# Kernel optimization log

Measured on AMD Instinct MI355X. Metric: run time of the kernel, lower is better.

## Reference

```python
import jax, jax.numpy as jnp
import numpy as np

B, N, E = 16, 64, 512
C_IMG = 512
H1, H2, H3 = 256, 128, 64
U, R = 8, 8
BBC = 9
EH1, EH2 = 64, 64
BBOX_POS_MAX = 1024.0
EPS = 1e-5


def setup_inputs():
    key = jax.random.key(0)
    ks = jax.random.split(key, 24)
    f = lambda i, shape, s=0.05: jax.random.normal(ks[i], shape, jnp.float32) * s
    return {
        'roi_features': f(0, (B, N, C_IMG), 1.0),
        'batch_bboxes': jax.random.uniform(ks[1], (B, N, 4)) * BBOX_POS_MAX,
        'batch_directions': jax.random.uniform(ks[2], (B, N, 4)),
        'batch_priorities': jax.random.uniform(ks[3], (B, N)),
        'w1': f(4, (C_IMG, H1)), 'b1': f(5, (H1,)),
        'bn1_g': jnp.ones((H1,)), 'bn1_b': jnp.zeros((H1,)),
        'bn1_m': jnp.zeros((H1,)), 'bn1_v': jnp.ones((H1,)),
        'w2': f(6, (H1, H2)), 'b2': f(7, (H2,)),
        'bn2_g': jnp.ones((H2,)), 'bn2_b': jnp.zeros((H2,)),
        'bn2_m': jnp.zeros((H2,)), 'bn2_v': jnp.ones((H2,)),
        'w3': f(8, (H2, H3)), 'b3': f(9, (H3,)),
        'wn': f(10, (H3, U)), 'bn_c': f(11, (U,)),
        'we1': f(12, (2 * BBC, EH1)), 'be1': f(13, (EH1,)),
        'we2': f(14, (EH1, EH2)), 'be2': f(15, (EH2,)),
        'wei': f(16, (EH2, R)), 'bei': f(17, (R,)),
        'edge_index': jax.random.randint(ks[18], (B, 2, E), 0, N, dtype=jnp.int32),
    }


def _bn(x, g, b, m, v):
    # BatchNorm1d in eval mode (running stats)
    return (x - m) * jax.lax.rsqrt(v + EPS) * g + b


def _build_see(edge_index):
    # Padded neighbor table replacing edge_index2dict:
    # see[b,n,0] = n, then srcs of edges with dst==n, in original edge order.
    src = edge_index[:, 0, :]                                   # [B,E]
    dst = edge_index[:, 1, :]                                   # [B,E]
    eq = dst[:, :, None] == dst[:, None, :]                     # [B,E,E]
    lower = jnp.tril(jnp.ones((E, E), bool), -1)
    pos = jnp.sum(eq & lower, axis=-1) + 1                      # rank within dst group, +1 for self slot
    see = jnp.zeros((B, N, N), jnp.int32).at[:, :, 0].set(jnp.arange(N, dtype=jnp.int32))
    b_idx = jnp.arange(B)[:, None]
    see = see.at[b_idx, dst, pos].set(src, mode='drop')
    deg = jnp.zeros((B, N), jnp.int32).at[b_idx, dst].add(1)
    count = jnp.minimum(deg + 1, N)
    mask = (jnp.arange(N)[None, None, :] < count[:, :, None]).astype(jnp.float32)  # [B,N,N]
    return see, mask


def _forward(roi_features, batch_bboxes, batch_directions, batch_priorities,
             w1, b1, bn1_g, bn1_b, bn1_m, bn1_v,
             w2, b2, bn2_g, bn2_b, bn2_m, bn2_v,
             w3, b3, wn, bn_c,
             we1, be1, we2, be2, wei, bei, edge_index):
    see, mask = _build_see(edge_index)
    # --- node branch (node_predictor + node_concept_interpreter) ---
    x = roi_features.reshape(B * N, C_IMG)
    x = jax.nn.relu(_bn(x @ w1 + b1, bn1_g, bn1_b, bn1_m, bn1_v))
    x = jax.nn.relu(_bn(x @ w2 + b2, bn2_g, bn2_b, bn2_m, bn2_v))
    x = jax.nn.relu(x @ w3 + b3)
    node_c = jax.nn.sigmoid(x @ wn + bn_c).reshape(B, N, U)
    # get_nlm_unary_concepts: gather per-node neighborhood into dense [B,N,N,U]
    gu = jax.vmap(lambda u, s: u[s])(node_c, see)               # [B,N,N,U]
    node_concepts = (gu * mask[..., None]).reshape(B * N, N, U)
    # --- edge branch ---
    attr = jnp.concatenate([batch_bboxes / BBOX_POS_MAX, batch_directions,
                            batch_priorities[..., None]], axis=-1)  # [B,N,BBC]
    pair = jnp.concatenate([
        jnp.broadcast_to(attr[:, :, None, :], (B, N, N, BBC)),
        jnp.broadcast_to(attr[:, None, :, :], (B, N, N, BBC))], axis=-1).reshape(-1, 2 * BBC)
    e = jax.nn.relu(pair @ we1 + be1)
    e = jax.nn.relu(e @ we2 + be2)
    rel = jax.nn.sigmoid(e @ wei + bei).reshape(B, N, N, R)
    # get_nlm_binary_concepts: rel[b, see[b,n,i], see[b,n,j]] with zero padding
    def per_b(r, s, m):
        g = r[s[:, :, None], s[:, None, :]]                     # [N,N,N,R]
        return g * (m[:, :, None, None] * m[:, None, :, None])
    edge_concepts = jax.vmap(per_b)(rel, see, mask).reshape(B * N, N, N, R)
    return node_concepts, edge_concepts


def reference(roi_features, batch_bboxes, batch_directions, batch_priorities,
              w1, b1, bn1_g, bn1_b, bn1_m, bn1_v,
              w2, b2, bn2_g, bn2_b, bn2_m, bn2_v,
              w3, b3, wn, bn_c,
              we1, be1, we2, be2, wei, bei, edge_index):
    return _forward(roi_features, batch_bboxes, batch_directions, batch_priorities,
                    w1, b1, bn1_g, bn1_b, bn1_m, bn1_v,
                    w2, b2, bn2_g, bn2_b, bn2_m, bn2_v,
                    w3, b3, wn, bn_c,
                    we1, be1, we2, be2, wei, bei, edge_index)
```

## Files before the change

### kernel.cpp

```cpp
#include <hip/hip_runtime.h>
#include <math.h>

#define BB    16
#define NN    64
#define EE    512
#define CIMG  512
#define H1D   256
#define H2D   128
#define H3D   64
#define UD    8
#define RD    8
#define BBCD  9
#define EH1D  64
#define EH2D  64
#define EPSF  1e-5f

typedef float nfloat4 __attribute__((ext_vector_type(4)));

__global__ __launch_bounds__(256) void fusedA_kernel(
    const int* __restrict__ edge_index,
    const float* __restrict__ bboxes,
    const float* __restrict__ dirs,
    const float* __restrict__ prios,
    const float* __restrict__ we1, const float* __restrict__ be1,
    int* __restrict__ see, int* __restrict__ cnt,
    const float* __restrict__ roi,
    const float* __restrict__ w1, const float* __restrict__ b1,
    const float* __restrict__ g1, const float* __restrict__ bt1,
    const float* __restrict__ m1, const float* __restrict__ v1,
    const float* __restrict__ w2, const float* __restrict__ b2,
    const float* __restrict__ g2, const float* __restrict__ bt2,
    const float* __restrict__ m2, const float* __restrict__ v2,
    const float* __restrict__ w3, const float* __restrict__ b3,
    const float* __restrict__ wn, const float* __restrict__ bnc,
    float* __restrict__ node_c,
    const float* __restrict__ we2, const float* __restrict__ be2,
    const float* __restrict__ wei, const float* __restrict__ bei,
    float* __restrict__ rel,
    float* __restrict__ out_edge)
{
    __shared__ union {
        struct {
            int src[EE];
            int dst[EE];
            int see[NN * NN];
        } p;
        struct {
            float part[4096];
            float h1[4][H1D];
            float h2[4][H2D];
            float h3[4][H3D];
        } n;
        struct {
            float e1[NN * 68];
            float qw[NN * EH1D];
            float wei[EH2D * RD];
            float attr[NN][BBCD];
            float we1[2 * BBCD * EH1D];
            float Pi[EH1D];
            float be2[EH2D];
            float bei[RD];
        } e;
    } sm;

    const int t = threadIdx.x;

    if (blockIdx.x >= BB + 256 + BB * NN) {
        const int id = blockIdx.x - (BB + 256 + BB * NN);
        nfloat4* dst = (nfloat4*)(out_edge + (size_t)id * NN * NN * RD);
        const nfloat4 z = {0.f, 0.f, 0.f, 0.f};
        #pragma unroll
        for (int it = 0; it < 16; ++it) {
            int task = it * 256 + t;
            __builtin_nontemporal_store(z, dst + task * 2);
            __builtin_nontemporal_store(z, dst + task * 2 + 1);
        }
        return;
    }

    if (blockIdx.x < BB) {
        const int b = blockIdx.x;
        const int* ei = edge_index + b * 2 * EE;
        for (int e = t; e < EE; e += 256) {
            sm.p.src[e] = ei[e];
            sm.p.dst[e] = ei[EE + e];
        }
        for (int x = t; x < NN * NN; x += 256)
            sm.p.see[x] = ((x & (NN - 1)) == 0) ? (x >> 6) : 0;
        __syncthreads();

        if (t < NN) {
            int pos = 0;
            #pragma unroll 8
            for (int e = 0; e < EE; ++e) {
                if (sm.p.dst[e] == t) {
                    ++pos;
                    if (pos < NN) sm.p.see[t * NN + pos] = sm.p.src[e];
                }
            }
            int c = pos + 1;
            cnt[b * NN + t] = (c < NN) ? c : NN;
        }
        __syncthreads();

        int4* dst4 = (int4*)(see + b * NN * NN);
        const int4* src4 = (const int4*)sm.p.see;
        for (int x = t; x < (NN * NN) / 4; x += 256) dst4[x] = src4[x];
        return;
    }

    if (blockIdx.x >= BB + 256) {
        const int id = blockIdx.x - (BB + 256);
        const int b = id >> 6;
        const int i = id & 63;

        if (t < NN) {
            const float* bbp = bboxes + (b * NN + t) * 4;
            const float* ddp = dirs + (b * NN + t) * 4;
            sm.e.attr[t][0] = bbp[0] * (1.0f / 1024.0f);
            sm.e.attr[t][1] = bbp[1] * (1.0f / 1024.0f);
            sm.e.attr[t][2] = bbp[2] * (1.0f / 1024.0f);
            sm.e.attr[t][3] = bbp[3] * (1.0f / 1024.0f);
            sm.e.attr[t][4] = ddp[0];
            sm.e.attr[t][5] = ddp[1];
            sm.e.attr[t][6] = ddp[2];
            sm.e.attr[t][7] = ddp[3];
            sm.e.attr[t][8] = prios[b * NN + t];
        }
        for (int x = t; x < 2 * BBCD * EH1D; x += 256) sm.e.we1[x] = we1[x];
        {
            const float4* w4 = (const float4*)we2;
            float4* qw4 = (float4*)sm.e.qw;
            #pragma unroll
            for (int x = 0; x < 4; ++x) qw4[x * 256 + t] = w4[x * 256 + t];
        }
        if (t < 128) ((float4*)sm.e.wei)[t] = ((const float4*)wei)[t];
        if (t < EH2D) sm.e.be2[t] = be2[t];
        if (t < RD) sm.e.bei[t] = bei[t];
        __syncthreads();

        if (t < EH1D) {
            float p = be1[t];
            #pragma unroll
            for (int c = 0; c < BBCD; ++c)
                p = fmaf(sm.e.attr[i][c], sm.e.we1[c * EH1D + t], p);
            sm.e.Pi[t] = p;
        }
        __syncthreads();

        {
            const int o = t & 63;
            const int jw = t >> 6;
            #pragma unroll
            for (int jg = 0; jg < 16; ++jg) {
                const int j = jg * 4 + jw;
                float a = sm.e.Pi[o];
                #pragma unroll
                for (int c = 0; c < BBCD; ++c)
                    a = fmaf(sm.e.attr[j][c], sm.e.we1[(BBCD + c) * EH1D + o], a);
                sm.e.e1[j * 68 + o] = fmaxf(0.f, a);
            }
        }
        __syncthreads();

        const int tx = t & 15, ty = t >> 4;
        const int o0 = tx * 4, j0 = ty * 4;
        float acc[4][4];
        #pragma unroll
        for (int r = 0; r < 4; ++r)
            #pragma unroll
            for (int o = 0; o < 4; ++o) acc[r][o] = 0.f;

        #pragma unroll 4
        for (int cg = 0; cg < 16; ++cg) {
            float ev[4][4];
            #pragma unroll
            for (int r = 0; r < 4; ++r) {
                float4 v = *(const float4*)(sm.e.e1 + (j0 + r) * 68 + cg * 4);
                ev[r][0] = v.x; ev[r][1] = v.y; ev[r][2] = v.z; ev[r][3] = v.w;
            }
            #pragma unroll
            for (int q = 0; q < 4; ++q) {
                float4 wv = *(const float4*)(sm.e.qw + (cg * 4 + q) * EH1D + o0);
                #pragma unroll
                for (int r = 0; r < 4; ++r) {
                    acc[r][0] = fmaf(ev[r][q], wv.x, acc[r][0]);
                    acc[r][1] = fmaf(ev[r][q], wv.y, acc[r][1]);
                    acc[r][2] = fmaf(ev[r][q], wv.z, acc[r][2]);
                    acc[r][3] = fmaf(ev[r][q], wv.w, acc[r][3]);
                }
            }
        }

        {
            float4 bv = *(const float4*)(sm.e.be2 + o0);
            #pragma unroll
            for (int r = 0; r < 4; ++r) {
                float4 v;
                v.x = fmaxf(0.f, acc[r][0] + bv.x);
                v.y = fmaxf(0.f, acc[r][1] + bv.y);
                v.z = fmaxf(0.f, acc[r][2] + bv.z);
                v.w = fmaxf(0.f, acc[r][3] + bv.w);
                *(float4*)(sm.e.e1 + (j0 + r) * 68 + o0) = v;
            }
        }
        __syncthreads();

        {
            const int j = t >> 2;
            const int r0 = (t & 3) * 2;
            float a0 = sm.e.bei[r0], a1 = sm.e.bei[r0 + 1];
            const float* e2row = sm.e.e1 + j * 68;
            #pragma unroll
            for (int og = 0; og < 16; ++og) {
                float4 e2v = *(const float4*)(e2row + og * 4);
                float2 w0 = *(const float2*)(sm.e.wei + (og * 4 + 0) * RD + r0);
                float2 w1 = *(const float2*)(sm.e.wei + (og * 4 + 1) * RD + r0);
                float2 w2 = *(const float2*)(sm.e.wei + (og * 4 + 2) * RD + r0);
                float2 w3 = *(const float2*)(sm.e.wei + (og * 4 + 3) * RD + r0);
                a0 = fmaf(e2v.x, w0.x, a0); a1 = fmaf(e2v.x, w0.y, a1);
                a0 = fmaf(e2v.y, w1.x, a0); a1 = fmaf(e2v.y, w1.y, a1);
                a0 = fmaf(e2v.z, w2.x, a0); a1 = fmaf(e2v.z, w2.y, a1);
                a0 = fmaf(e2v.w, w3.x, a0); a1 = fmaf(e2v.w, w3.y, a1);
            }
            float2 o;
            o.x = 1.f / (1.f + expf(-a0));
            o.y = 1.f / (1.f + expf(-a1));
            *(float2*)(rel + ((size_t)id * NN + j) * RD + r0) = o;
        }
        return;
    }

    const int row0 = (blockIdx.x - BB) * 4;
    float* part = sm.n.part;

    {
        const int og = t & 63, kg = t >> 6;
        const float4* w1v = (const float4*)w1;
        const float4* roiv = (const float4*)(roi + (size_t)row0 * CIMG);
        float acc[4][4];
        #pragma unroll
        for (int r = 0; r < 4; ++r)
            #pragma unroll
            for (int c = 0; c < 4; ++c) acc[r][c] = 0.f;

        for (int cq = 0; cq < 32; ++cq) {
            const int c4 = kg * 32 + cq;
            float x[4][4], w[4][4];
            #pragma unroll
            for (int r = 0; r < 4; ++r) {
                float4 v = roiv[r * 128 + c4];
                x[r][0] = v.x; x[r][1] = v.y; x[r][2] = v.z; x[r][3] = v.w;
            }
            #pragma unroll
            for (int q = 0; q < 4; ++q) {
                float4 v = w1v[(size_t)(c4 * 4 + q) * 64 + og];
                w[q][0] = v.x; w[q][1] = v.y; w[q][2] = v.z; w[q][3] = v.w;
            }
            #pragma unroll
            for (int r = 0; r < 4; ++r)
                #pragma unroll
                for (int q = 0; q < 4; ++q)
                    #pragma unroll
                    for (int c = 0; c < 4; ++c)
                        acc[r][c] = fmaf(x[r][q], w[q][c], acc[r][c]);
        }
        #pragma unroll
        for (int r = 0; r < 4; ++r) {
            float4 v = {acc[r][0], acc[r][1], acc[r][2], acc[r][3]};
            *(float4*)(part + (kg * 4 + r) * 256 + og * 4) = v;
        }
    }
    __syncthreads();
    {
        const int o = t;
        const float bias = b1[o];
        const float scale = rsqrtf(v1[o] + EPSF) * g1[o];
        const float beta = bt1[o];
        const float mu = m1[o];
        #pragma unroll
        for (int r = 0; r < 4; ++r) {
            float s = part[(0 * 4 + r) * 256 + o] + part[(1 * 4 + r) * 256 + o]
                    + part[(2 * 4 + r) * 256 + o] + part[(3 * 4 + r) * 256 + o];
            sm.n.h1[r][o] = fmaxf(0.f, (s + bias - mu) * scale + beta);
        }
    }
    __syncthreads();

    {
        const int og = t & 31, kg = t >> 5;
        const float4* w2v = (const float4*)w2;
        float acc[4][4];
        #pragma unroll
        for (int r = 0; r < 4; ++r)
            #pragma unroll
            for (int c = 0; c < 4; ++c) acc[r][c] = 0.f;

        #pragma unroll
        for (int cq = 0; cq < 8; ++cq) {
            const int c4 = kg * 8 + cq;
            float x[4][4], w[4][4];
            #pragma unroll
            for (int r = 0; r < 4; ++r) {
                float4 v = *(const float4*)&sm.n.h1[r][c4 * 4];
                x[r][0] = v.x; x[r][1] = v.y; x[r][2] = v.z; x[r][3] = v.w;
            }
            #pragma unroll
            for (int q = 0; q < 4; ++q) {
                float4 v = w2v[(size_t)(c4 * 4 + q) * 32 + og];
                w[q][0] = v.x; w[q][1] = v.y; w[q][2] = v.z; w[q][3] = v.w;
            }
            #pragma unroll
            for (int r = 0; r < 4; ++r)
                #pragma unroll
                for (int q = 0; q < 4; ++q)
                    #pragma unroll
                    for (int c = 0; c < 4; ++c)
                        acc[r][c] = fmaf(x[r][q], w[q][c], acc[r][c]);
        }
        #pragma unroll
        for (int r = 0; r < 4; ++r) {
            float4 v = {acc[r][0], acc[r][1], acc[r][2], acc[r][3]};
            *(float4*)(part + (kg * 4 + r) * 128 + og * 4) = v;
        }
    }
    __syncthreads();
    {
        const int o = t & 127;
        const int rp = t >> 7;
        const float bias = b2[o];
        const float scale = rsqrtf(v2[o] + EPSF) * g2[o];
        const float beta = bt2[o];
        const float mu = m2[o];
        #pragma unroll
        for (int rr = 0; rr < 2; ++rr) {
            const int r = rp + rr * 2;
            float s = 0.f;
            #pragma unroll
            for (int kg = 0; kg < 8; ++kg) s += part[(kg * 4 + r) * 128 + o];
            sm.n.h2[r][o] = fmaxf(0.f, (s + bias - mu) * scale + beta);
        }
    }
    __syncthreads();

    {
        const int og = t & 15, kg = t >> 4;
        const float4* w3v = (const float4*)w3;
        float acc[4][4];
        #pragma unroll
        for (int r = 0; r < 4; ++r)
            #pragma unroll
            for (int c = 0; c < 4; ++c) acc[r][c] = 0.f;

        #pragma unroll
        for (int cq = 0; cq < 2; ++cq) {
            const int c4 = kg * 2 + cq;
            float x[4][4], w[4][4];
            #pragma unroll
            for (int r = 0; r < 4; ++r) {
                float4 v = *(const float4*)&sm.n.h2[r][c4 * 4];
                x[r][0] = v.x; x[r][1] = v.y; x[r][2] = v.z; x[r][3] = v.w;
            }
            #pragma unroll
            for (int q = 0; q < 4; ++q) {
                float4 v = w3v[(size_t)(c4 * 4 + q) * 16 + og];
                w[q][0] = v.x; w[q][1] = v.y; w[q][2] = v.z; w[q][3] = v.w;
            }
            #pragma unroll
            for (int r = 0; r < 4; ++r)
                #pragma unroll
                for (int q = 0; q < 4; ++q)
                    #pragma unroll
                    for (int c = 0; c < 4; ++c)
                        acc[r][c] = fmaf(x[r][q], w[q][c], acc[r][c]);
        }
        #pragma unroll
        for (int r = 0; r < 4; ++r) {
            float4 v = {acc[r][0], acc[r][1], acc[r][2], acc[r][3]};
            *(float4*)(part + (kg * 4 + r) * 64 + og * 4) = v;
        }
    }
    __syncthreads();
    {
        const int o = t & 63;
        const int r = t >> 6;
        float s = b3[o];
        #pragma unroll
        for (int kg = 0; kg < 16; ++kg) s += part[(kg * 4 + r) * 64 + o];
        sm.n.h3[r][o] = fmaxf(0.f, s);
    }
    __syncthreads();

    if (t < 32) {
        const int o = t & 7, r = t >> 3;
        float a = bnc[o];
        #pragma unroll 8
        for (int c = 0; c < H3D; ++c) a = fmaf(sm.n.h3[r][c], wn[c * UD + o], a);
        node_c[(size_t)(row0 + r) * UD + o] = 1.f / (1.f + expf(-a));
    }
}

__global__ __launch_bounds__(256) void gather_kernel(
    const int* __restrict__ see, const int* __restrict__ cnt,
    const float* __restrict__ node_c, const float* __restrict__ rel,
    float* __restrict__ out_node, float* __restrict__ out_edge)
{
    __shared__ int s_s[NN];

    const int t = threadIdx.x;
    const int bi = blockIdx.x;
    const int b = bi >> 6;
    const int c = cnt[bi];

    if (t < NN) s_s[t] = see[bi * NN + t];
    __syncthreads();

    if (t < NN) {
        const float m = (t < c) ? 1.f : 0.f;
        const float4* src = (const float4*)(node_c + (size_t)(b * NN + s_s[t]) * UD);
        float4 v0 = src[0], v1 = src[1];
        v0.x *= m; v0.y *= m; v0.z *= m; v0.w *= m;
        v1.x *= m; v1.y *= m; v1.z *= m; v1.w *= m;
        float4* dst = (float4*)(out_node + ((size_t)bi * NN + t) * UD);
        dst[0] = v0;
        dst[1] = v1;
    }

    const float* relb = rel + (size_t)b * NN * NN * RD;
    float* outb = out_edge + (size_t)bi * NN * NN * RD;

    const int total = c * c;
    for (int task = t; task < total; task += 256) {
        int j = task / c;
        int k = task - j * c;
        const float4* src =
            (const float4*)(relb + (size_t)(s_s[j] * NN + s_s[k]) * RD);
        float4 v0 = src[0], v1 = src[1];
        float4* dst = (float4*)(outb + ((size_t)j * NN + k) * RD);
        dst[0] = v0;
        dst[1] = v1;
    }
}

extern "C" void kernel_launch(void* const* d_in, const int* in_sizes, int n_in,
                              void* d_out, int out_size, void* d_ws, size_t ws_size,
                              hipStream_t stream)
{
    const float* roi  = (const float*)d_in[0];
    const float* bbox = (const float*)d_in[1];
    const float* dirs = (const float*)d_in[2];
    const float* prio = (const float*)d_in[3];
    const float* w1   = (const float*)d_in[4];
    const float* b1   = (const float*)d_in[5];
    const float* g1   = (const float*)d_in[6];
    const float* bt1  = (const float*)d_in[7];
    const float* m1   = (const float*)d_in[8];
    const float* v1   = (const float*)d_in[9];
    const float* w2   = (const float*)d_in[10];
    const float* b2   = (const float*)d_in[11];
    const float* g2   = (const float*)d_in[12];
    const float* bt2  = (const float*)d_in[13];
    const float* m2   = (const float*)d_in[14];
    const float* v2   = (const float*)d_in[15];
    const float* w3   = (const float*)d_in[16];
    const float* b3   = (const float*)d_in[17];
    const float* wn   = (const float*)d_in[18];
    const float* bnc  = (const float*)d_in[19];
    const float* we1  = (const float*)d_in[20];
    const float* be1  = (const float*)d_in[21];
    const float* we2  = (const float*)d_in[22];
    const float* be2  = (const float*)d_in[23];
    const float* wei  = (const float*)d_in[24];
    const float* bei  = (const float*)d_in[25];
    const int* edge_index = (const int*)d_in[26];

    char* ws = (char*)d_ws;
    int*   see    = (int*)ws;   ws += (size_t)BB * NN * NN * 4;
    int*   cnt    = (int*)ws;   ws += (size_t)BB * NN * 4;
    float* node_c = (float*)ws; ws += (size_t)BB * NN * UD * 4;
    float* rel    = (float*)ws; ws += (size_t)BB * NN * NN * RD * 4;

    float* out_node = (float*)d_out;
    float* out_edge = (float*)d_out + (size_t)BB * NN * NN * UD;

    hipLaunchKernelGGL(fusedA_kernel,
                       dim3(BB + 256 + BB * NN + BB * NN), dim3(256), 0, stream,
                       edge_index, bbox, dirs, prio, we1, be1,
                       see, cnt,
                       roi, w1, b1, g1, bt1, m1, v1,
                       w2, b2, g2, bt2, m2, v2,
                       w3, b3, wn, bnc, node_c,
                       we2, be2, wei, bei, rel, out_edge);
    hipLaunchKernelGGL(gather_kernel, dim3(BB * NN), dim3(256), 0, stream,
                       see, cnt, node_c, rel, out_node, out_edge);
}
```

Measured before the change: 261.2 us.

## Merge zero-fill of edge output into gather kernel to write each element once

Removes the separate zero-fill blocks from the first kernel and has the gather kernel write every output edge element exactly once, either gathered relation values or zeros. This avoids the double write of the valid region and the extra grid blocks. The cost is that the large zero-fill can no longer overlap with the first kernel's compute, since it now runs after it.

```diff
diff --git a/kernel.cpp b/kernel.cpp
--- a/kernel.cpp
+++ b/kernel.cpp
@@ -36,8 +36,7 @@
     float* __restrict__ node_c,
     const float* __restrict__ we2, const float* __restrict__ be2,
     const float* __restrict__ wei, const float* __restrict__ bei,
-    float* __restrict__ rel,
-    float* __restrict__ out_edge)
+    float* __restrict__ rel)
 {
     __shared__ union {
         struct {
@@ -65,19 +64,6 @@
 
     const int t = threadIdx.x;
 
-    if (blockIdx.x >= BB + 256 + BB * NN) {
-        const int id = blockIdx.x - (BB + 256 + BB * NN);
-        nfloat4* dst = (nfloat4*)(out_edge + (size_t)id * NN * NN * RD);
-        const nfloat4 z = {0.f, 0.f, 0.f, 0.f};
-        #pragma unroll
-        for (int it = 0; it < 16; ++it) {
-            int task = it * 256 + t;
-            __builtin_nontemporal_store(z, dst + task * 2);
-            __builtin_nontemporal_store(z, dst + task * 2 + 1);
-        }
-        return;
-    }
-
     if (blockIdx.x < BB) {
         const int b = blockIdx.x;
         const int* ei = edge_index + b * 2 * EE;
@@ -400,7 +386,7 @@
     }
 }
 
-__global__ __launch_bounds__(256) void gather_kernel(
+__global__ __launch_bounds__(256) void gatherfill_kernel(
     const int* __restrict__ see, const int* __restrict__ cnt,
     const float* __restrict__ node_c, const float* __restrict__ rel,
     float* __restrict__ out_node, float* __restrict__ out_edge)
@@ -428,17 +414,29 @@
 
     const float* relb = rel + (size_t)b * NN * NN * RD;
     float* outb = out_edge + (size_t)bi * NN * NN * RD;
-
-    const int total = c * c;
-    for (int task = t; task < total; task += 256) {
-        int j = task / c;
-        int k = task - j * c;
-        const float4* src =
-            (const float4*)(relb + (size_t)(s_s[j] * NN + s_s[k]) * RD);
-        float4 v0 = src[0], v1 = src[1];
-        float4* dst = (float4*)(outb + ((size_t)j * NN + k) * RD);
-        dst[0] = v0;
-        dst[1] = v1;
+    const nfloat4 z = {0.f, 0.f, 0.f, 0.f};
+
+    #pragma unroll
+    for (int it = 0; it < (NN * NN) / 256; ++it) {
+        const int task = it * 256 + t;
+        const int j = task >> 6;
+        const int k = task & 63;
+        nfloat4* dst = (nfloat4*)(outb + (size_t)task * RD);
+        if (j < c) {
+            if (k < c) {
+                const float4* src =
+                    (const float4*)(relb + (size_t)(s_s[j] * NN + s_s[k]) * RD);
+                float4 v0 = src[0], v1 = src[1];
+                ((float4*)dst)[0] = v0;
+                ((float4*)dst)[1] = v1;
+            } else {
+                __builtin_nontemporal_store(z, dst);
+                __builtin_nontemporal_store(z, dst + 1);
+            }
+        } else {
+            __builtin_nontemporal_store(z, dst);
+            __builtin_nontemporal_store(z, dst + 1);
+        }
     }
 }
 
@@ -484,13 +482,13 @@
     float* out_edge = (float*)d_out + (size_t)BB * NN * NN * UD;
 
     hipLaunchKernelGGL(fusedA_kernel,
-                       dim3(BB + 256 + BB * NN + BB * NN), dim3(256), 0, stream,
+                       dim3(BB + 256 + BB * NN), dim3(256), 0, stream,
                        edge_index, bbox, dirs, prio, we1, be1,
                        see, cnt,
                        roi, w1, b1, g1, bt1, m1, v1,
                        w2, b2, g2, bt2, m2, v2,
                        w3, b3, wn, bnc, node_c,
-                       we2, be2, wei, bei, rel, out_edge);
-    hipLaunchKernelGGL(gather_kernel, dim3(BB * NN), dim3(256), 0, stream,
+                       we2, be2, wei, bei, rel);
+    hipLaunchKernelGGL(gatherfill_kernel, dim3(BB * NN), dim3(256), 0, stream,
                        see, cnt, node_c, rel, out_node, out_edge);
 }
```

Result: faster. 249.4 us (-4.5%).
